# Kernel optimization log

Hardware: AMD Instinct MI355X
Metric: run time of the kernel (lower is better)

## Reference

```python
import jax, jax.numpy as jnp
import numpy as np

N_HEADS = 16
D_MODEL = 1024
NEG_INF = float('-inf')


def _rope_tables(seq_len, d_k, dtype):
    # RoPE(dim=d_k//2): Theta_i = 10000^(-i/dim), repeat-interleaved to width d_k;
    # positions start at 1 (torch uses arange(1, max_len+1)).
    dim = d_k // 2
    theta = jnp.exp(-jnp.arange(dim, dtype=dtype) * (np.log(10000.0) / dim))
    theta = jnp.repeat(theta, 2)                      # [d_k]
    pos = jnp.arange(1, seq_len + 1, dtype=dtype)[:, None]  # [S,1]
    ang = pos * theta                                 # [S,d_k]
    return jnp.sin(ang), jnp.cos(ang)


def _rope(x):
    # x: [B,H,S,d_k]; pair rotation (x0,x1)->(-x1,x0), Rx = x*cos + rot(x)*sin
    B, H, S, d_k = x.shape
    sin, cos = _rope_tables(S, d_k, x.dtype)
    xp = x.reshape(B, H, S, d_k // 2, 2)
    rot = jnp.stack([-xp[..., 1], xp[..., 0]], axis=-1).reshape(x.shape)
    return x * cos + rot * sin


def setup_inputs() -> dict:
    key = jax.random.key(0)
    ks = jax.random.split(key, 8)
    B, S, D, H = 2, 1024, D_MODEL, N_HEADS
    source_query = jax.random.normal(ks[0], (B, S, D), dtype=jnp.float32)
    source_key_value = jax.random.normal(ks[1], (B, S, D), dtype=jnp.float32)
    # tail padding: lengths in [820, 1024]
    q_len = jax.random.randint(ks[2], (B,), 820, S + 1)
    kv_len = jax.random.randint(ks[3], (B,), 820, S + 1)
    pos = jnp.arange(S)
    source_query_padding_mask = pos[None, :] >= q_len[:, None]    # True = pad
    source_key_value_padding_mask = pos[None, :] >= kv_len[:, None]
    prev = jax.random.normal(ks[4], (1, B, H, S, S), dtype=jnp.float32) * 0.5
    Wq = jax.random.normal(ks[5], (D, D), dtype=jnp.float32) * 0.02
    Wk = jax.random.normal(ks[6], (D, D), dtype=jnp.float32) * 0.02
    kv2 = jax.random.split(ks[7], 2)
    Wv = jax.random.normal(kv2[0], (D, D), dtype=jnp.float32) * 0.02
    Wproj = jax.random.normal(kv2[1], (D, D), dtype=jnp.float32) * 0.02
    return dict(source_query=source_query, source_key_value=source_key_value,
                source_query_padding_mask=source_query_padding_mask,
                source_key_value_padding_mask=source_key_value_padding_mask,
                prev=prev, Wq=Wq, Wk=Wk, Wv=Wv, Wproj=Wproj)


def reference(source_query, source_key_value, source_query_padding_mask,
              source_key_value_padding_mask, prev, Wq, Wk, Wv, Wproj):
    B, Sq, D = source_query.shape
    Sk = source_key_value.shape[1]
    H = N_HEADS
    d_k = D // H

    def split_heads(x, S):
        return x.reshape(B, S, H, d_k).transpose(0, 2, 1, 3)  # [B,H,S,d_k]

    # nn.Linear(bias=False): y = x @ W.T
    q = split_heads(jnp.einsum('bsd,ed->bse', source_query, Wq), Sq)
    k = split_heads(jnp.einsum('bsd,ed->bse', source_key_value, Wk), Sk)
    v = split_heads(jnp.einsum('bsd,ed->bse', source_key_value, Wv), Sk)

    q = _rope(q)
    k = _rope(k)

    scores = jnp.einsum('bhqd,bhkd->bhqk', q, k) * (d_k ** -0.5)
    q_pad = source_query_padding_mask[:, None, :, None]   # [B,1,Sq,1]
    kv_pad = source_key_value_padding_mask[:, None, None, :]  # [B,1,1,Sk]
    scores = jnp.where(q_pad, NEG_INF, scores)
    scores = jnp.where(kv_pad, NEG_INF, scores)
    causal = jnp.tril(jnp.ones((Sq, Sq), dtype=bool))      # masked=True
    scores = jnp.where(causal, scores, NEG_INF)

    prev_new = jnp.concatenate([prev, scores[None]], axis=0)  # [L+1,B,H,Sq,Sk]
    avg = prev_new.mean(0)

    # rows fully -inf (padded queries) would softmax to NaN in torch, then get
    # filled with 0 -> compute a safe softmax and zero those rows instead.
    safe = jnp.where(q_pad, 0.0, avg)
    w = jax.nn.softmax(safe, axis=-1)
    w = jnp.where(q_pad, 0.0, w)

    attn = jnp.einsum('bhqk,bhkd->bhqd', w, v)
    attn = attn.transpose(0, 2, 1, 3).reshape(B, Sq, D)
    out = jnp.einsum('bsd,ed->bse', attn, Wproj)  # dropout=0 (eval)
    return out, prev_new
```

## Files before the change

kernel.cpp:

```cpp
#include <hip/hip_runtime.h>
#include <math.h>

#define NSEQ 1024
#define NH   16
#define DKH  64

#define NEGBIG (-1.0e30f)

typedef unsigned short u16;
typedef unsigned int   u32;
typedef __attribute__((ext_vector_type(8))) short short8;
typedef __attribute__((ext_vector_type(4))) float f32x4;

__global__ __launch_bounds__(256) void normalize_masks(
    const unsigned char* __restrict__ qm, const unsigned char* __restrict__ km,
    int* __restrict__ outq, int* __restrict__ outk)
{
    __shared__ int flag;
    if (threadIdx.x == 0) flag = 0;
    __syncthreads();
    int f = 0;
    for (int i = threadIdx.x; i < 2048; i += 256) {
        if ((i & 3) && qm[i]) f = 1;
        if ((i & 3) && km[i]) f = 1;
    }
    if (f) atomicOr(&flag, 1);
    __syncthreads();
    const int isbyte = flag;
    for (int i = threadIdx.x; i < 2048; i += 256) {
        outq[i] = isbyte ? (int)qm[i] : ((const int*)qm)[i];
        outk[i] = isbyte ? (int)km[i] : ((const int*)km)[i];
    }
}

__device__ __forceinline__ u32 bf16_rn(float x) {
    u32 u = __float_as_uint(x);
    return (u + 0x7FFFu + ((u >> 16) & 1u)) >> 16;
}
__device__ __forceinline__ void bf16_split(float x, u32 &h, u32 &l) {
    h = bf16_rn(x);
    l = bf16_rn(x - __uint_as_float(h << 16));
}

__global__ __launch_bounds__(256) void split_bf16(
    const float* __restrict__ srcq, const float* __restrict__ srckv,
    const float* __restrict__ Wq, const float* __restrict__ Wk,
    const float* __restrict__ Wv, const float* __restrict__ Wp,
    u16* __restrict__ sqh, u16* __restrict__ sql,
    u16* __restrict__ skvh, u16* __restrict__ skvl,
    u16* __restrict__ w4h, u16* __restrict__ w4l)
{
    const int z = blockIdx.z;
    const float* src; u16 *dh, *dl; int n;
    if (z == 0)      { src = srcq;  dh = sqh;  dl = sql;  n = 1 << 21; }
    else if (z == 1) { src = srckv; dh = skvh; dl = skvl; n = 1 << 21; }
    else {
        src = (z == 2) ? Wq : (z == 3) ? Wk : (z == 4) ? Wv : Wp;
        dh = w4h + ((size_t)(z - 2) << 20);
        dl = w4l + ((size_t)(z - 2) << 20);
        n = 1 << 20;
    }
    const int i8 = (blockIdx.x * 256 + threadIdx.x) * 8;
    if (i8 >= n) return;
    const float4 a = *(const float4*)&src[i8];
    const float4 b = *(const float4*)&src[i8 + 4];
    const float v[8] = {a.x, a.y, a.z, a.w, b.x, b.y, b.z, b.w};
    u32 h[8], l[8];
    #pragma unroll
    for (int j = 0; j < 8; ++j) bf16_split(v[j], h[j], l[j]);
    *(uint4*)&dh[i8] = make_uint4(h[0] | (h[1] << 16), h[2] | (h[3] << 16),
                                  h[4] | (h[5] << 16), h[6] | (h[7] << 16));
    *(uint4*)&dl[i8] = make_uint4(l[0] | (l[1] << 16), l[2] | (l[3] << 16),
                                  l[4] | (l[5] << 16), l[6] | (l[7] << 16));
}

__global__ __launch_bounds__(256) void full_copy(
    const float* __restrict__ prev, float* __restrict__ prevc,
    float* __restrict__ scb)
{
    const float4 n4 = make_float4(NEGBIG, NEGBIG, NEGBIG, NEGBIG);
    for (unsigned i = blockIdx.x * 256 + threadIdx.x; i < (1u << 23); i += gridDim.x * 256) {
        const size_t e = (size_t)i * 4;
        const float4 p = *(const float4*)&prev[e];
        *(float4*)&prevc[e] = p;
        const int q = (int)((e >> 10) & 1023);
        const int k = (int)(e & 1023);
        if ((k >> 6) > (q >> 6)) *(float4*)&scb[e] = n4;
    }
}

__device__ __forceinline__ void mfma_core(
    const u16* __restrict__ Xhi, const u16* __restrict__ Xlo,
    const u16* __restrict__ Whi, const u16* __restrict__ Wlo,
    u16 (*Ahi)[40], u16 (*Alo)[40], u16 (*Bhi)[40], u16 (*Blo)[40],
    f32x4 (&acc)[4][2], int m0, int e0, int tid)
{
    const int lane = tid & 63, wid = tid >> 6;
    const int wm = wid >> 1, wn = wid & 1;
    const int l15 = lane & 15, lq = lane >> 4;
    const int arow = tid >> 1, aks = (tid & 1) * 16;
    const int brow = tid >> 2, bks = (tid & 3) * 8;
    const u16* axh = &Xhi[(size_t)(m0 + arow) * 1024 + aks];
    const u16* axl = &Xlo[(size_t)(m0 + arow) * 1024 + aks];
    const u16* bxh = &Whi[(size_t)(e0 + brow) * 1024 + bks];
    const u16* bxl = &Wlo[(size_t)(e0 + brow) * 1024 + bks];

    uint4 rah0 = *(const uint4*)axh;
    uint4 rah1 = *(const uint4*)(axh + 8);
    uint4 ral0 = *(const uint4*)axl;
    uint4 ral1 = *(const uint4*)(axl + 8);
    uint4 rbh  = *(const uint4*)bxh;
    uint4 rbl  = *(const uint4*)bxl;

    for (int k0 = 0; k0 < 1024; k0 += 32) {
        __syncthreads();
        *(uint4*)&Ahi[arow][aks]     = rah0;
        *(uint4*)&Ahi[arow][aks + 8] = rah1;
        *(uint4*)&Alo[arow][aks]     = ral0;
        *(uint4*)&Alo[arow][aks + 8] = ral1;
        *(uint4*)&Bhi[brow][bks]     = rbh;
        *(uint4*)&Blo[brow][bks]     = rbl;
        __syncthreads();
        if (k0 + 32 < 1024) {
            rah0 = *(const uint4*)(axh + k0 + 32);
            rah1 = *(const uint4*)(axh + k0 + 40);
            ral0 = *(const uint4*)(axl + k0 + 32);
            ral1 = *(const uint4*)(axl + k0 + 40);
            rbh  = *(const uint4*)(bxh + k0 + 32);
            rbl  = *(const uint4*)(bxl + k0 + 32);
        }
        short8 bh8[2], bl8[2];
        #pragma unroll
        for (int fn = 0; fn < 2; ++fn) {
            const int bc = wn * 32 + fn * 16 + l15;
            bh8[fn] = *(const short8*)&Bhi[bc][lq * 8];
            bl8[fn] = *(const short8*)&Blo[bc][lq * 8];
        }
        #pragma unroll
        for (int fm = 0; fm < 4; ++fm) {
            const int ar = wm * 64 + fm * 16 + l15;
            short8 ah8 = *(const short8*)&Ahi[ar][lq * 8];
            short8 al8 = *(const short8*)&Alo[ar][lq * 8];
            #pragma unroll
            for (int fn = 0; fn < 2; ++fn) {
                acc[fm][fn] = __builtin_amdgcn_mfma_f32_16x16x32_bf16(ah8, bh8[fn], acc[fm][fn], 0, 0, 0);
                acc[fm][fn] = __builtin_amdgcn_mfma_f32_16x16x32_bf16(ah8, bl8[fn], acc[fm][fn], 0, 0, 0);
                acc[fm][fn] = __builtin_amdgcn_mfma_f32_16x16x32_bf16(al8, bh8[fn], acc[fm][fn], 0, 0, 0);
            }
        }
    }
}

__global__ __launch_bounds__(256) void gemm_qkv(
    const u16* __restrict__ sqh, const u16* __restrict__ sql,
    const u16* __restrict__ skvh, const u16* __restrict__ skvl,
    const u16* __restrict__ w4h, const u16* __restrict__ w4l,
    float* __restrict__ qh, float* __restrict__ kh, float* __restrict__ vh)
{
    __shared__ __align__(16) u16 Ahi[128][40];
    __shared__ __align__(16) u16 Alo[128][40];
    __shared__ __align__(16) u16 Bhi[64][40];
    __shared__ __align__(16) u16 Blo[64][40];
    const int tid = threadIdx.x;
    const int z = blockIdx.z;
    const u16* Xhi = (z == 0) ? sqh : skvh;
    const u16* Xlo = (z == 0) ? sql : skvl;
    const u16* Whi = w4h + ((size_t)z << 20);
    const u16* Wlo = w4l + ((size_t)z << 20);
    float* Y = (z == 0) ? qh : (z == 1) ? kh : vh;
    const int m0 = blockIdx.y * 128, e0 = blockIdx.x * 64;

    f32x4 acc[4][2];
    #pragma unroll
    for (int i = 0; i < 4; ++i)
        #pragma unroll
        for (int j = 0; j < 2; ++j) acc[i][j] = (f32x4){0.f, 0.f, 0.f, 0.f};

    mfma_core(Xhi, Xlo, Whi, Wlo, Ahi, Alo, Bhi, Blo, acc, m0, e0, tid);

    const int lane = tid & 63, wid = tid >> 6;
    const int wm = wid >> 1, wn = wid & 1;
    const int l15 = lane & 15, lq = lane >> 4;
    const bool rope = (z != 2);
    const float cth = 0.28782313662425575f;
    float th[2];
    #pragma unroll
    for (int fn = 0; fn < 2; ++fn) {
        const int e = e0 + wn * 32 + fn * 16 + l15;
        th[fn] = rope ? expf(-(float)((e & 63) >> 1) * cth) : 0.f;
    }
    #pragma unroll
    for (int fm = 0; fm < 4; ++fm) {
        #pragma unroll
        for (int r = 0; r < 4; ++r) {
            const int m = m0 + wm * 64 + fm * 16 + lq * 4 + r;
            const int b = m >> 10, s = m & 1023;
            const float pos = (float)(s + 1);
            #pragma unroll
            for (int fn = 0; fn < 2; ++fn) {
                const int e = e0 + wn * 32 + fn * 16 + l15;
                float v = acc[fm][fn][r];
                const float vp = __shfl_xor(v, 1);
                if (rope) {
                    float sp, cp;
                    sincosf(pos * th[fn], &sp, &cp);
                    v = (lane & 1) ? (v * cp + vp * sp) : (v * cp - vp * sp);
                }
                const int hh = e >> 6, db = e & 63;
                Y[(((size_t)(b * NH + hh) << 10) + s) * DKH + db] = v;
            }
        }
    }
}

__global__ __launch_bounds__(256) void gemm_proj(
    const u16* __restrict__ atnh, const u16* __restrict__ atnl,
    const u16* __restrict__ wph, const u16* __restrict__ wpl,
    float* __restrict__ Y)
{
    __shared__ __align__(16) u16 Ahi[128][40];
    __shared__ __align__(16) u16 Alo[128][40];
    __shared__ __align__(16) u16 Bhi[64][40];
    __shared__ __align__(16) u16 Blo[64][40];
    const int tid = threadIdx.x;
    const int m0 = blockIdx.y * 128, e0 = blockIdx.x * 64;

    f32x4 acc[4][2];
    #pragma unroll
    for (int i = 0; i < 4; ++i)
        #pragma unroll
        for (int j = 0; j < 2; ++j) acc[i][j] = (f32x4){0.f, 0.f, 0.f, 0.f};

    mfma_core(atnh, atnl, wph, wpl, Ahi, Alo, Bhi, Blo, acc, m0, e0, tid);

    const int lane = tid & 63, wid = tid >> 6;
    const int wm = wid >> 1, wn = wid & 1;
    const int l15 = lane & 15, lq = lane >> 4;
    #pragma unroll
    for (int fm = 0; fm < 4; ++fm) {
        #pragma unroll
        for (int fn = 0; fn < 2; ++fn) {
            #pragma unroll
            for (int r = 0; r < 4; ++r) {
                const int row = m0 + wm * 64 + fm * 16 + lq * 4 + r;
                const int col = e0 + wn * 32 + fn * 16 + l15;
                Y[(size_t)row * 1024 + col] = acc[fm][fn][r];
            }
        }
    }
}

__global__ __launch_bounds__(256) void flash_fused(
    const float* __restrict__ qh, const float* __restrict__ kh,
    const float* __restrict__ vh, const float* __restrict__ prev,
    const int* __restrict__ nmq, const int* __restrict__ nmk,
    float* __restrict__ scb, u16* __restrict__ atnh, u16* __restrict__ atnl)
{
    const int bh = blockIdx.y;
    const int b = bh >> 4, h = bh & 15;
    const int bx = blockIdx.x;
    const int qt = (bx & 1) ? (15 - (bx >> 1)) : (bx >> 1);
    const int q0 = qt * 64;
    const int tid = threadIdx.x;
    const int ti = tid >> 4, tj = tid & 15;
    const int r0 = ti * 4, c0 = tj * 4;
    const size_t base = ((size_t)bh << 10) * 1024;
    const float NI = NEGBIG;

    __shared__ float Qs[64][68];
    __shared__ float KW[64][68];
    __shared__ float Vs[64][68];

    const int lr = tid >> 2;
    const int ld0 = (tid & 3) * 4;
    {
        const float* qbase = qh + (((size_t)bh << 10) + q0) * DKH;
        #pragma unroll
        for (int dq = 0; dq < 4; ++dq) {
            const int d0 = ld0 + dq * 16;
            float4 qv = *(const float4*)&qbase[(size_t)lr * DKH + d0];
            Qs[d0 + 0][lr] = qv.x; Qs[d0 + 1][lr] = qv.y;
            Qs[d0 + 2][lr] = qv.z; Qs[d0 + 3][lr] = qv.w;
        }
    }

    int qmv[4];
    #pragma unroll
    for (int i = 0; i < 4; ++i) qmv[i] = nmq[(b << 10) + q0 + r0 + i];

    float m_i[4], l_i[4], O[4][4];
    #pragma unroll
    for (int i = 0; i < 4; ++i) {
        m_i[i] = -3.0e38f; l_i[i] = 0.f;
        #pragma unroll
        for (int j = 0; j < 4; ++j) O[i][j] = 0.f;
    }

    const float* kbase = kh + ((size_t)bh << 10) * DKH;
    const float* vbase = vh + ((size_t)bh << 10) * DKH;

    for (int kt = 0; kt <= qt; ++kt) {
        const int k0 = kt * 64;
        __syncthreads();

        #pragma unroll
        for (int dq = 0; dq < 4; ++dq) {
            const int d0 = ld0 + dq * 16;
            float4 kv4 = *(const float4*)&kbase[(size_t)(k0 + lr) * DKH + d0];
            KW[d0 + 0][lr] = kv4.x; KW[d0 + 1][lr] = kv4.y;
            KW[d0 + 2][lr] = kv4.z; KW[d0 + 3][lr] = kv4.w;
        }
        #pragma unroll
        for (int u = 0; u < 4; ++u) {
            const int e = u * 256 + tid;
            const int kv = e >> 4, dd = (e & 15) * 4;
            *(float4*)&Vs[kv][dd] =
                *(const float4*)&vbase[(size_t)(k0 + kv) * DKH + dd];
        }
        __syncthreads();

        float acc[4][4] = {{0.f}};
        #pragma unroll 8
        for (int d = 0; d < 64; ++d) {
            float a[4], bb[4];
            *(float4*)a  = *(const float4*)&Qs[d][r0];
            *(float4*)bb = *(const float4*)&KW[d][c0];
            #pragma unroll
            for (int i = 0; i < 4; ++i)
                #pragma unroll
                for (int j = 0; j < 4; ++j)
                    acc[i][j] += a[i] * bb[j];
        }

        int km[4];
        #pragma unroll
        for (int j = 0; j < 4; ++j) km[j] = nmk[(b << 10) + k0 + c0 + j];
        float aw[4][4], tmx[4];
        #pragma unroll
        for (int i = 0; i < 4; ++i) {
            const int row = q0 + r0 + i;
            float o[4];
            #pragma unroll
            for (int j = 0; j < 4; ++j) {
                const int col = k0 + c0 + j;
                const bool masked = (col > row) || (qmv[i] != 0) || (km[j] != 0);
                o[j] = masked ? NI : acc[i][j] * 0.125f;
            }
            const size_t idx = base + (size_t)row * 1024 + k0 + c0;
            *(float4*)&scb[idx] = make_float4(o[0], o[1], o[2], o[3]);
            const float4 p4 = *(const float4*)&prev[idx];
            aw[i][0] = 0.5f * (p4.x + o[0]);
            aw[i][1] = 0.5f * (p4.y + o[1]);
            aw[i][2] = 0.5f * (p4.z + o[2]);
            aw[i][3] = 0.5f * (p4.w + o[3]);
            tmx[i] = fmaxf(fmaxf(aw[i][0], aw[i][1]), fmaxf(aw[i][2], aw[i][3]));
        }
        #pragma unroll
        for (int i = 0; i < 4; ++i)
            #pragma unroll
            for (int off = 1; off < 16; off <<= 1)
                tmx[i] = fmaxf(tmx[i], __shfl_xor(tmx[i], off));

        __syncthreads();

        #pragma unroll
        for (int i = 0; i < 4; ++i) {
            const float mn = fmaxf(m_i[i], tmx[i]);
            const float fac = expf(m_i[i] - mn);
            m_i[i] = mn;
            float w0 = expf(aw[i][0] - mn);
            float w1 = expf(aw[i][1] - mn);
            float w2 = expf(aw[i][2] - mn);
            float w3 = expf(aw[i][3] - mn);
            float sl = w0 + w1 + w2 + w3;
            #pragma unroll
            for (int off = 1; off < 16; off <<= 1)
                sl += __shfl_xor(sl, off);
            l_i[i] = l_i[i] * fac + sl;
            #pragma unroll
            for (int j = 0; j < 4; ++j) O[i][j] *= fac;
            KW[c0 + 0][r0 + i] = w0;
            KW[c0 + 1][r0 + i] = w1;
            KW[c0 + 2][r0 + i] = w2;
            KW[c0 + 3][r0 + i] = w3;
        }
        __syncthreads();

        #pragma unroll 8
        for (int k = 0; k < 64; ++k) {
            float wv[4], vv[4];
            *(float4*)wv = *(const float4*)&KW[k][r0];
            *(float4*)vv = *(const float4*)&Vs[k][c0];
            #pragma unroll
            for (int i = 0; i < 4; ++i)
                #pragma unroll
                for (int j = 0; j < 4; ++j)
                    O[i][j] += wv[i] * vv[j];
        }
    }

    #pragma unroll
    for (int i = 0; i < 4; ++i) {
        const int q = q0 + r0 + i;
        const float inv = qmv[i] ? 0.f : 1.f / l_i[i];
        u32 sh0, sl0, sh1, sl1, sh2, sl2, sh3, sl3;
        bf16_split(O[i][0] * inv, sh0, sl0);
        bf16_split(O[i][1] * inv, sh1, sl1);
        bf16_split(O[i][2] * inv, sh2, sl2);
        bf16_split(O[i][3] * inv, sh3, sl3);
        const size_t aidx = (size_t)((b << 10) + q) * 1024 + (h << 6) + c0;
        *(uint2*)&atnh[aidx] = make_uint2(sh0 | (sh1 << 16), sh2 | (sh3 << 16));
        *(uint2*)&atnl[aidx] = make_uint2(sl0 | (sl1 << 16), sl2 | (sl3 << 16));
    }
}

extern "C" void kernel_launch(void* const* d_in, const int* in_sizes, int n_in,
                              void* d_out, int out_size, void* d_ws, size_t ws_size,
                              hipStream_t stream) {
    const float* srcq  = (const float*)d_in[0];
    const float* srckv = (const float*)d_in[1];
    const void*  qmask = d_in[2];
    const void*  kmask = d_in[3];
    const float* prev  = (const float*)d_in[4];
    const float* Wq    = (const float*)d_in[5];
    const float* Wk    = (const float*)d_in[6];
    const float* Wv    = (const float*)d_in[7];
    const float* Wp    = (const float*)d_in[8];

    float* out0  = (float*)d_out;
    float* prevc = out0 + 2097152;
    float* scb   = prevc + 33554432;

    float* qh   = (float*)d_ws;
    float* kh   = qh + 2097152;
    float* vh   = kh + 2097152;
    u16* atnh = (u16*)(vh + 2097152);
    u16* atnl = atnh + 2097152;
    u16* sqh  = atnl + 2097152;
    u16* sql  = sqh + 2097152;
    u16* skvh = sql + 2097152;
    u16* skvl = skvh + 2097152;
    u16* w4h  = skvl + 2097152;
    u16* w4l  = w4h + 4194304;
    int* nmq  = (int*)(w4l + 4194304);
    int* nmk  = nmq + 2048;

    hipLaunchKernelGGL(normalize_masks, dim3(1), dim3(256), 0, stream,
                       (const unsigned char*)qmask, (const unsigned char*)kmask, nmq, nmk);
    hipLaunchKernelGGL(split_bf16, dim3(1024, 1, 6), dim3(256), 0, stream,
                       srcq, srckv, Wq, Wk, Wv, Wp,
                       sqh, sql, skvh, skvl, w4h, w4l);
    hipLaunchKernelGGL(gemm_qkv, dim3(16, 16, 3), dim3(256), 0, stream,
                       sqh, sql, skvh, skvl, w4h, w4l, qh, kh, vh);
    hipLaunchKernelGGL(full_copy, dim3(2048), dim3(256), 0, stream,
                       prev, prevc, scb);
    hipLaunchKernelGGL(flash_fused, dim3(16, 32), dim3(256), 0, stream,
                       qh, kh, vh, prev, nmq, nmk, scb, atnh, atnl);
    hipLaunchKernelGGL(gemm_proj, dim3(16, 16), dim3(256), 0, stream,
                       atnh, atnl, w4h + 3145728, w4l + 3145728, out0);
}
```

Before: 648.0 us.

## Pack GEMM operands into MFMA fragment order and fuse prev copy into attention

The bf16 split kernel now writes activations and weights in a pre-swizzled MFMA fragment layout. Both GEMMs use 128x128 tiles fed by double-buffered global_load_lds, running three sequential K passes (hi·hi, lo·hi, hi·lo) instead of interleaving three MFMAs per step. The separate full_copy kernel is removed: the attention kernel copies prev and writes the -inf score blocks for its own upper-triangle tiles. Each attention block now handles a complementary pair of query tiles to balance causal work, and writes its output already packed for the projection GEMM. The gain is less memory traffic and fewer launches, at the cost of tighter coupling between producer and consumer layouts and more work per attention block.

```diff
diff --git a/kernel.cpp b/kernel.cpp
--- a/kernel.cpp
+++ b/kernel.cpp
@@ -11,6 +11,12 @@
 typedef unsigned int   u32;
 typedef __attribute__((ext_vector_type(8))) short short8;
 typedef __attribute__((ext_vector_type(4))) float f32x4;
+
+__device__ __forceinline__ void gload_lds16(const void* g, void* l) {
+    __builtin_amdgcn_global_load_lds(
+        (const __attribute__((address_space(1))) void*)g,
+        (__attribute__((address_space(3))) void*)l, 16, 0, 0);
+}
 
 __global__ __launch_bounds__(256) void normalize_masks(
     const unsigned char* __restrict__ qm, const unsigned char* __restrict__ km,
@@ -42,7 +48,7 @@
     l = bf16_rn(x - __uint_as_float(h << 16));
 }
 
-__global__ __launch_bounds__(256) void split_bf16(
+__global__ __launch_bounds__(256) void split_pack(
     const float* __restrict__ srcq, const float* __restrict__ srckv,
     const float* __restrict__ Wq, const float* __restrict__ Wk,
     const float* __restrict__ Wv, const float* __restrict__ Wp,
@@ -51,103 +57,80 @@
     u16* __restrict__ w4h, u16* __restrict__ w4l)
 {
     const int z = blockIdx.z;
-    const float* src; u16 *dh, *dl; int n;
-    if (z == 0)      { src = srcq;  dh = sqh;  dl = sql;  n = 1 << 21; }
-    else if (z == 1) { src = srckv; dh = skvh; dl = skvl; n = 1 << 21; }
+    const float* src; u16 *dh, *dl; int nunits;
+    if (z == 0)      { src = srcq;  dh = sqh;  dl = sql;  nunits = 262144; }
+    else if (z == 1) { src = srckv; dh = skvh; dl = skvl; nunits = 262144; }
     else {
         src = (z == 2) ? Wq : (z == 3) ? Wk : (z == 4) ? Wv : Wp;
         dh = w4h + ((size_t)(z - 2) << 20);
         dl = w4l + ((size_t)(z - 2) << 20);
-        n = 1 << 20;
-    }
-    const int i8 = (blockIdx.x * 256 + threadIdx.x) * 8;
-    if (i8 >= n) return;
-    const float4 a = *(const float4*)&src[i8];
-    const float4 b = *(const float4*)&src[i8 + 4];
-    const float v[8] = {a.x, a.y, a.z, a.w, b.x, b.y, b.z, b.w};
-    u32 h[8], l[8];
+        nunits = 131072;
+    }
+    const int u = blockIdx.x * 256 + threadIdx.x;
+    if (u >= nunits) return;
+    const int lane = u & 63, kstep = (u >> 6) & 31, sub = u >> 11;
+    const int row = sub * 16 + (lane & 15);
+    const int kc  = kstep * 32 + ((lane >> 4) << 3);
+    const float4 a = *(const float4*)&src[(size_t)row * 1024 + kc];
+    const float4 bb = *(const float4*)&src[(size_t)row * 1024 + kc + 4];
+    const float v[8] = {a.x, a.y, a.z, a.w, bb.x, bb.y, bb.z, bb.w};
+    u32 hh[8], ll[8];
     #pragma unroll
-    for (int j = 0; j < 8; ++j) bf16_split(v[j], h[j], l[j]);
-    *(uint4*)&dh[i8] = make_uint4(h[0] | (h[1] << 16), h[2] | (h[3] << 16),
-                                  h[4] | (h[5] << 16), h[6] | (h[7] << 16));
-    *(uint4*)&dl[i8] = make_uint4(l[0] | (l[1] << 16), l[2] | (l[3] << 16),
-                                  l[4] | (l[5] << 16), l[6] | (l[7] << 16));
-}
-
-__global__ __launch_bounds__(256) void full_copy(
-    const float* __restrict__ prev, float* __restrict__ prevc,
-    float* __restrict__ scb)
-{
-    const float4 n4 = make_float4(NEGBIG, NEGBIG, NEGBIG, NEGBIG);
-    for (unsigned i = blockIdx.x * 256 + threadIdx.x; i < (1u << 23); i += gridDim.x * 256) {
-        const size_t e = (size_t)i * 4;
-        const float4 p = *(const float4*)&prev[e];
-        *(float4*)&prevc[e] = p;
-        const int q = (int)((e >> 10) & 1023);
-        const int k = (int)(e & 1023);
-        if ((k >> 6) > (q >> 6)) *(float4*)&scb[e] = n4;
-    }
-}
-
-__device__ __forceinline__ void mfma_core(
-    const u16* __restrict__ Xhi, const u16* __restrict__ Xlo,
-    const u16* __restrict__ Whi, const u16* __restrict__ Wlo,
-    u16 (*Ahi)[40], u16 (*Alo)[40], u16 (*Bhi)[40], u16 (*Blo)[40],
-    f32x4 (&acc)[4][2], int m0, int e0, int tid)
+    for (int j = 0; j < 8; ++j) bf16_split(v[j], hh[j], ll[j]);
+    const size_t o = (size_t)u * 8;
+    *(uint4*)&dh[o] = make_uint4(hh[0] | (hh[1] << 16), hh[2] | (hh[3] << 16),
+                                 hh[4] | (hh[5] << 16), hh[6] | (hh[7] << 16));
+    *(uint4*)&dl[o] = make_uint4(ll[0] | (ll[1] << 16), ll[2] | (ll[3] << 16),
+                                 ll[4] | (ll[5] << 16), ll[6] | (ll[7] << 16));
+}
+
+__device__ __forceinline__ void gemm_packed_core(
+    const u16* __restrict__ Ah, const u16* __restrict__ Al,
+    const u16* __restrict__ Bh, const u16* __restrict__ Bl,
+    u16* LA, u16* LB, f32x4 (&acc)[4][4], int m0, int e0, int tid)
 {
     const int lane = tid & 63, wid = tid >> 6;
     const int wm = wid >> 1, wn = wid & 1;
-    const int l15 = lane & 15, lq = lane >> 4;
-    const int arow = tid >> 1, aks = (tid & 1) * 16;
-    const int brow = tid >> 2, bks = (tid & 3) * 8;
-    const u16* axh = &Xhi[(size_t)(m0 + arow) * 1024 + aks];
-    const u16* axl = &Xlo[(size_t)(m0 + arow) * 1024 + aks];
-    const u16* bxh = &Whi[(size_t)(e0 + brow) * 1024 + bks];
-    const u16* bxl = &Wlo[(size_t)(e0 + brow) * 1024 + bks];
-
-    uint4 rah0 = *(const uint4*)axh;
-    uint4 rah1 = *(const uint4*)(axh + 8);
-    uint4 ral0 = *(const uint4*)axl;
-    uint4 ral1 = *(const uint4*)(axl + 8);
-    uint4 rbh  = *(const uint4*)bxh;
-    uint4 rbl  = *(const uint4*)bxl;
-
-    for (int k0 = 0; k0 < 1024; k0 += 32) {
+    const int subA0 = m0 >> 4, subB0 = e0 >> 4;
+    const int s0 = wid, s1 = wid + 4;
+    const int lo8 = lane * 8;
+
+    int cur = 0;
+    gload_lds16(Ah + ((size_t)(subA0 + s0) * 32) * 512 + lo8, LA + s0 * 512);
+    gload_lds16(Ah + ((size_t)(subA0 + s1) * 32) * 512 + lo8, LA + s1 * 512);
+    gload_lds16(Bh + ((size_t)(subB0 + s0) * 32) * 512 + lo8, LB + s0 * 512);
+    gload_lds16(Bh + ((size_t)(subB0 + s1) * 32) * 512 + lo8, LB + s1 * 512);
+    __syncthreads();
+
+    for (int ks = 0; ks < 96; ++ks) {
+        const int nxt = ks + 1;
+        if (nxt < 96) {
+            const int kstep = nxt & 31, ph = nxt >> 5;
+            const u16* Ap = (ph == 1) ? Al : Ah;
+            const u16* Bp = (ph == 2) ? Bl : Bh;
+            u16* la = LA + (cur ^ 1) * 4096;
+            u16* lb = LB + (cur ^ 1) * 4096;
+            gload_lds16(Ap + ((size_t)(subA0 + s0) * 32 + kstep) * 512 + lo8, la + s0 * 512);
+            gload_lds16(Ap + ((size_t)(subA0 + s1) * 32 + kstep) * 512 + lo8, la + s1 * 512);
+            gload_lds16(Bp + ((size_t)(subB0 + s0) * 32 + kstep) * 512 + lo8, lb + s0 * 512);
+            gload_lds16(Bp + ((size_t)(subB0 + s1) * 32 + kstep) * 512 + lo8, lb + s1 * 512);
+        }
+        const u16* la = LA + cur * 4096;
+        const u16* lb = LB + cur * 4096;
+        short8 a8[4], b8[4];
+        #pragma unroll
+        for (int f = 0; f < 4; ++f) {
+            a8[f] = *(const short8*)(la + (wm * 4 + f) * 512 + lo8);
+            b8[f] = *(const short8*)(lb + (wn * 4 + f) * 512 + lo8);
+        }
+        #pragma unroll
+        for (int fm = 0; fm < 4; ++fm)
+            #pragma unroll
+            for (int fn = 0; fn < 4; ++fn)
+                acc[fm][fn] = __builtin_amdgcn_mfma_f32_16x16x32_bf16(
+                    a8[fm], b8[fn], acc[fm][fn], 0, 0, 0);
         __syncthreads();
-        *(uint4*)&Ahi[arow][aks]     = rah0;
-        *(uint4*)&Ahi[arow][aks + 8] = rah1;
-        *(uint4*)&Alo[arow][aks]     = ral0;
-        *(uint4*)&Alo[arow][aks + 8] = ral1;
-        *(uint4*)&Bhi[brow][bks]     = rbh;
-        *(uint4*)&Blo[brow][bks]     = rbl;
-        __syncthreads();
-        if (k0 + 32 < 1024) {
-            rah0 = *(const uint4*)(axh + k0 + 32);
-            rah1 = *(const uint4*)(axh + k0 + 40);
-            ral0 = *(const uint4*)(axl + k0 + 32);
-            ral1 = *(const uint4*)(axl + k0 + 40);
-            rbh  = *(const uint4*)(bxh + k0 + 32);
-            rbl  = *(const uint4*)(bxl + k0 + 32);
-        }
-        short8 bh8[2], bl8[2];
-        #pragma unroll
-        for (int fn = 0; fn < 2; ++fn) {
-            const int bc = wn * 32 + fn * 16 + l15;
-            bh8[fn] = *(const short8*)&Bhi[bc][lq * 8];
-            bl8[fn] = *(const short8*)&Blo[bc][lq * 8];
-        }
-        #pragma unroll
-        for (int fm = 0; fm < 4; ++fm) {
-            const int ar = wm * 64 + fm * 16 + l15;
-            short8 ah8 = *(const short8*)&Ahi[ar][lq * 8];
-            short8 al8 = *(const short8*)&Alo[ar][lq * 8];
-            #pragma unroll
-            for (int fn = 0; fn < 2; ++fn) {
-                acc[fm][fn] = __builtin_amdgcn_mfma_f32_16x16x32_bf16(ah8, bh8[fn], acc[fm][fn], 0, 0, 0);
-                acc[fm][fn] = __builtin_amdgcn_mfma_f32_16x16x32_bf16(ah8, bl8[fn], acc[fm][fn], 0, 0, 0);
-                acc[fm][fn] = __builtin_amdgcn_mfma_f32_16x16x32_bf16(al8, bh8[fn], acc[fm][fn], 0, 0, 0);
-            }
-        }
+        cur ^= 1;
     }
 }
 
@@ -157,56 +140,48 @@
     const u16* __restrict__ w4h, const u16* __restrict__ w4l,
     float* __restrict__ qh, float* __restrict__ kh, float* __restrict__ vh)
 {
-    __shared__ __align__(16) u16 Ahi[128][40];
-    __shared__ __align__(16) u16 Alo[128][40];
-    __shared__ __align__(16) u16 Bhi[64][40];
-    __shared__ __align__(16) u16 Blo[64][40];
+    __shared__ __align__(16) u16 LA[2][4096];
+    __shared__ __align__(16) u16 LB[2][4096];
     const int tid = threadIdx.x;
     const int z = blockIdx.z;
-    const u16* Xhi = (z == 0) ? sqh : skvh;
-    const u16* Xlo = (z == 0) ? sql : skvl;
-    const u16* Whi = w4h + ((size_t)z << 20);
-    const u16* Wlo = w4l + ((size_t)z << 20);
+    const u16* Ah = (z == 0) ? sqh : skvh;
+    const u16* Al = (z == 0) ? sql : skvl;
+    const u16* Bh = w4h + ((size_t)z << 20);
+    const u16* Bl = w4l + ((size_t)z << 20);
     float* Y = (z == 0) ? qh : (z == 1) ? kh : vh;
-    const int m0 = blockIdx.y * 128, e0 = blockIdx.x * 64;
-
-    f32x4 acc[4][2];
+    const int m0 = blockIdx.y * 128, e0 = blockIdx.x * 128;
+
+    f32x4 acc[4][4];
     #pragma unroll
     for (int i = 0; i < 4; ++i)
         #pragma unroll
-        for (int j = 0; j < 2; ++j) acc[i][j] = (f32x4){0.f, 0.f, 0.f, 0.f};
-
-    mfma_core(Xhi, Xlo, Whi, Wlo, Ahi, Alo, Bhi, Blo, acc, m0, e0, tid);
+        for (int j = 0; j < 4; ++j) acc[i][j] = (f32x4){0.f, 0.f, 0.f, 0.f};
+
+    gemm_packed_core(Ah, Al, Bh, Bl, &LA[0][0], &LB[0][0], acc, m0, e0, tid);
 
     const int lane = tid & 63, wid = tid >> 6;
     const int wm = wid >> 1, wn = wid & 1;
     const int l15 = lane & 15, lq = lane >> 4;
     const bool rope = (z != 2);
     const float cth = 0.28782313662425575f;
-    float th[2];
     #pragma unroll
-    for (int fn = 0; fn < 2; ++fn) {
-        const int e = e0 + wn * 32 + fn * 16 + l15;
-        th[fn] = rope ? expf(-(float)((e & 63) >> 1) * cth) : 0.f;
-    }
-    #pragma unroll
-    for (int fm = 0; fm < 4; ++fm) {
-        #pragma unroll
-        for (int r = 0; r < 4; ++r) {
-            const int m = m0 + wm * 64 + fm * 16 + lq * 4 + r;
-            const int b = m >> 10, s = m & 1023;
-            const float pos = (float)(s + 1);
-            #pragma unroll
-            for (int fn = 0; fn < 2; ++fn) {
-                const int e = e0 + wn * 32 + fn * 16 + l15;
+    for (int fn = 0; fn < 4; ++fn) {
+        const int e = e0 + wn * 64 + fn * 16 + l15;
+        const float th = expf(-(float)((e & 63) >> 1) * cth);
+        const int hh = e >> 6, db = e & 63;
+        #pragma unroll
+        for (int fm = 0; fm < 4; ++fm) {
+            #pragma unroll
+            for (int r = 0; r < 4; ++r) {
+                const int m = m0 + wm * 64 + fm * 16 + lq * 4 + r;
+                const int b = m >> 10, s = m & 1023;
                 float v = acc[fm][fn][r];
                 const float vp = __shfl_xor(v, 1);
                 if (rope) {
                     float sp, cp;
-                    sincosf(pos * th[fn], &sp, &cp);
+                    sincosf((float)(s + 1) * th, &sp, &cp);
                     v = (lane & 1) ? (v * cp + vp * sp) : (v * cp - vp * sp);
                 }
-                const int hh = e >> 6, db = e & 63;
                 Y[(((size_t)(b * NH + hh) << 10) + s) * DKH + db] = v;
             }
         }
@@ -218,49 +193,44 @@
     const u16* __restrict__ wph, const u16* __restrict__ wpl,
     float* __restrict__ Y)
 {
-    __shared__ __align__(16) u16 Ahi[128][40];
-    __shared__ __align__(16) u16 Alo[128][40];
-    __shared__ __align__(16) u16 Bhi[64][40];
-    __shared__ __align__(16) u16 Blo[64][40];
+    __shared__ __align__(16) u16 LA[2][4096];
+    __shared__ __align__(16) u16 LB[2][4096];
     const int tid = threadIdx.x;
-    const int m0 = blockIdx.y * 128, e0 = blockIdx.x * 64;
-
-    f32x4 acc[4][2];
+    const int m0 = blockIdx.y * 128, e0 = blockIdx.x * 128;
+
+    f32x4 acc[4][4];
     #pragma unroll
     for (int i = 0; i < 4; ++i)
         #pragma unroll
-        for (int j = 0; j < 2; ++j) acc[i][j] = (f32x4){0.f, 0.f, 0.f, 0.f};
-
-    mfma_core(atnh, atnl, wph, wpl, Ahi, Alo, Bhi, Blo, acc, m0, e0, tid);
+        for (int j = 0; j < 4; ++j) acc[i][j] = (f32x4){0.f, 0.f, 0.f, 0.f};
+
+    gemm_packed_core(atnh, atnl, wph, wpl, &LA[0][0], &LB[0][0], acc, m0, e0, tid);
 
     const int lane = tid & 63, wid = tid >> 6;
     const int wm = wid >> 1, wn = wid & 1;
     const int l15 = lane & 15, lq = lane >> 4;
     #pragma unroll
-    for (int fm = 0; fm < 4; ++fm) {
-        #pragma unroll
-        for (int fn = 0; fn < 2; ++fn) {
+    for (int fm = 0; fm < 4; ++fm)
+        #pragma unroll
+        for (int fn = 0; fn < 4; ++fn)
             #pragma unroll
             for (int r = 0; r < 4; ++r) {
                 const int row = m0 + wm * 64 + fm * 16 + lq * 4 + r;
-                const int col = e0 + wn * 32 + fn * 16 + l15;
+                const int col = e0 + wn * 64 + fn * 16 + l15;
                 Y[(size_t)row * 1024 + col] = acc[fm][fn][r];
             }
-        }
-    }
 }
 
 __global__ __launch_bounds__(256) void flash_fused(
     const float* __restrict__ qh, const float* __restrict__ kh,
     const float* __restrict__ vh, const float* __restrict__ prev,
     const int* __restrict__ nmq, const int* __restrict__ nmk,
-    float* __restrict__ scb, u16* __restrict__ atnh, u16* __restrict__ atnl)
+    float* __restrict__ prevc, float* __restrict__ scb,
+    u16* __restrict__ atnh, u16* __restrict__ atnl)
 {
     const int bh = blockIdx.y;
     const int b = bh >> 4, h = bh & 15;
     const int bx = blockIdx.x;
-    const int qt = (bx & 1) ? (15 - (bx >> 1)) : (bx >> 1);
-    const int q0 = qt * 64;
     const int tid = threadIdx.x;
     const int ti = tid >> 4, tj = tid & 15;
     const int r0 = ti * 4, c0 = tj * 4;
@@ -273,144 +243,180 @@
 
     const int lr = tid >> 2;
     const int ld0 = (tid & 3) * 4;
-    {
-        const float* qbase = qh + (((size_t)bh << 10) + q0) * DKH;
-        #pragma unroll
-        for (int dq = 0; dq < 4; ++dq) {
-            const int d0 = ld0 + dq * 16;
-            float4 qv = *(const float4*)&qbase[(size_t)lr * DKH + d0];
-            Qs[d0 + 0][lr] = qv.x; Qs[d0 + 1][lr] = qv.y;
-            Qs[d0 + 2][lr] = qv.z; Qs[d0 + 3][lr] = qv.w;
-        }
-    }
-
-    int qmv[4];
-    #pragma unroll
-    for (int i = 0; i < 4; ++i) qmv[i] = nmq[(b << 10) + q0 + r0 + i];
-
-    float m_i[4], l_i[4], O[4][4];
-    #pragma unroll
-    for (int i = 0; i < 4; ++i) {
-        m_i[i] = -3.0e38f; l_i[i] = 0.f;
-        #pragma unroll
-        for (int j = 0; j < 4; ++j) O[i][j] = 0.f;
-    }
-
     const float* kbase = kh + ((size_t)bh << 10) * DKH;
     const float* vbase = vh + ((size_t)bh << 10) * DKH;
 
-    for (int kt = 0; kt <= qt; ++kt) {
-        const int k0 = kt * 64;
+    for (int pp = 0; pp < 2; ++pp) {
+        const int qt = pp ? (15 - bx) : bx;
+        const int q0 = qt * 64;
+
+        {
+            const float* qbase = qh + (((size_t)bh << 10) + q0) * DKH;
+            #pragma unroll
+            for (int dq = 0; dq < 4; ++dq) {
+                const int d0 = ld0 + dq * 16;
+                float4 qv = *(const float4*)&qbase[(size_t)lr * DKH + d0];
+                Qs[d0 + 0][lr] = qv.x; Qs[d0 + 1][lr] = qv.y;
+                Qs[d0 + 2][lr] = qv.z; Qs[d0 + 3][lr] = qv.w;
+            }
+        }
+
+        {
+            const float4 n4 = make_float4(NI, NI, NI, NI);
+            for (int kt = qt + 1; kt < 16; ++kt) {
+                const int k0 = kt * 64;
+                #pragma unroll
+                for (int u = 0; u < 4; ++u) {
+                    const int e = u * 256 + tid;
+                    const int rr = e >> 4, cc = (e & 15) * 4;
+                    const size_t idx = base + (size_t)(q0 + rr) * 1024 + k0 + cc;
+                    *(float4*)&prevc[idx] = *(const float4*)&prev[idx];
+                    *(float4*)&scb[idx] = n4;
+                }
+            }
+        }
+
+        int qmv[4];
+        #pragma unroll
+        for (int i = 0; i < 4; ++i) qmv[i] = nmq[(b << 10) + q0 + r0 + i];
+
+        float m_i[4], l_i[4], O[4][4];
+        #pragma unroll
+        for (int i = 0; i < 4; ++i) {
+            m_i[i] = -3.0e38f; l_i[i] = 0.f;
+            #pragma unroll
+            for (int j = 0; j < 4; ++j) O[i][j] = 0.f;
+        }
+
+        for (int kt = 0; kt <= qt; ++kt) {
+            const int k0 = kt * 64;
+            __syncthreads();
+
+            #pragma unroll
+            for (int dq = 0; dq < 4; ++dq) {
+                const int d0 = ld0 + dq * 16;
+                float4 kv4 = *(const float4*)&kbase[(size_t)(k0 + lr) * DKH + d0];
+                KW[d0 + 0][lr] = kv4.x; KW[d0 + 1][lr] = kv4.y;
+                KW[d0 + 2][lr] = kv4.z; KW[d0 + 3][lr] = kv4.w;
+            }
+            #pragma unroll
+            for (int u = 0; u < 4; ++u) {
+                const int e = u * 256 + tid;
+                const int kv = e >> 4, dd = (e & 15) * 4;
+                *(float4*)&Vs[kv][dd] =
+                    *(const float4*)&vbase[(size_t)(k0 + kv) * DKH + dd];
+            }
+            __syncthreads();
+
+            float acc[4][4] = {{0.f}};
+            #pragma unroll 8
+            for (int d = 0; d < 64; ++d) {
+                float a[4], bb[4];
+                *(float4*)a  = *(const float4*)&Qs[d][r0];
+                *(float4*)bb = *(const float4*)&KW[d][c0];
+                #pragma unroll
+                for (int i = 0; i < 4; ++i)
+                    #pragma unroll
+                    for (int j = 0; j < 4; ++j)
+                        acc[i][j] += a[i] * bb[j];
+            }
+
+            int km[4];
+            #pragma unroll
+            for (int j = 0; j < 4; ++j) km[j] = nmk[(b << 10) + k0 + c0 + j];
+            float aw[4][4], tmx[4];
+            #pragma unroll
+            for (int i = 0; i < 4; ++i) {
+                const int row = q0 + r0 + i;
+                float o[4];
+                #pragma unroll
+                for (int j = 0; j < 4; ++j) {
+                    const int col = k0 + c0 + j;
+                    const bool masked = (col > row) || (qmv[i] != 0) || (km[j] != 0);
+                    o[j] = masked ? NI : acc[i][j] * 0.125f;
+                }
+                const size_t idx = base + (size_t)row * 1024 + k0 + c0;
+                *(float4*)&scb[idx] = make_float4(o[0], o[1], o[2], o[3]);
+                const float4 p4 = *(const float4*)&prev[idx];
+                *(float4*)&prevc[idx] = p4;
+                aw[i][0] = 0.5f * (p4.x + o[0]);
+                aw[i][1] = 0.5f * (p4.y + o[1]);
+                aw[i][2] = 0.5f * (p4.z + o[2]);
+                aw[i][3] = 0.5f * (p4.w + o[3]);
+                tmx[i] = fmaxf(fmaxf(aw[i][0], aw[i][1]), fmaxf(aw[i][2], aw[i][3]));
+            }
+            #pragma unroll
+            for (int i = 0; i < 4; ++i)
+                #pragma unroll
+                for (int off = 1; off < 16; off <<= 1)
+                    tmx[i] = fmaxf(tmx[i], __shfl_xor(tmx[i], off));
+
+            __syncthreads();
+
+            #pragma unroll
+            for (int i = 0; i < 4; ++i) {
+                const float mn = fmaxf(m_i[i], tmx[i]);
+                const float fac = expf(m_i[i] - mn);
+                m_i[i] = mn;
+                float w0 = expf(aw[i][0] - mn);
+                float w1 = expf(aw[i][1] - mn);
+                float w2 = expf(aw[i][2] - mn);
+                float w3 = expf(aw[i][3] - mn);
+                float sl = w0 + w1 + w2 + w3;
+                #pragma unroll
+                for (int off = 1; off < 16; off <<= 1)
+                    sl += __shfl_xor(sl, off);
+                l_i[i] = l_i[i] * fac + sl;
+                #pragma unroll
+                for (int j = 0; j < 4; ++j) O[i][j] *= fac;
+                KW[c0 + 0][r0 + i] = w0;
+                KW[c0 + 1][r0 + i] = w1;
+                KW[c0 + 2][r0 + i] = w2;
+                KW[c0 + 3][r0 + i] = w3;
+            }
+            __syncthreads();
+
+            #pragma unroll 8
+            for (int k = 0; k < 64; ++k) {
+                float wv[4], vv[4];
+                *(float4*)wv = *(const float4*)&KW[k][r0];
+                *(float4*)vv = *(const float4*)&Vs[k][c0];
+                #pragma unroll
+                for (int i = 0; i < 4; ++i)
+                    #pragma unroll
+                    for (int j = 0; j < 4; ++j)
+                        O[i][j] += wv[i] * vv[j];
+            }
+        }
+
         __syncthreads();
-
-        #pragma unroll
-        for (int dq = 0; dq < 4; ++dq) {
-            const int d0 = ld0 + dq * 16;
-            float4 kv4 = *(const float4*)&kbase[(size_t)(k0 + lr) * DKH + d0];
-            KW[d0 + 0][lr] = kv4.x; KW[d0 + 1][lr] = kv4.y;
-            KW[d0 + 2][lr] = kv4.z; KW[d0 + 3][lr] = kv4.w;
-        }
-        #pragma unroll
-        for (int u = 0; u < 4; ++u) {
-            const int e = u * 256 + tid;
-            const int kv = e >> 4, dd = (e & 15) * 4;
-            *(float4*)&Vs[kv][dd] =
-                *(const float4*)&vbase[(size_t)(k0 + kv) * DKH + dd];
+        #pragma unroll
+        for (int i = 0; i < 4; ++i) {
+            const float inv = qmv[i] ? 0.f : 1.f / l_i[i];
+            KW[r0 + i][c0 + 0] = O[i][0] * inv;
+            KW[r0 + i][c0 + 1] = O[i][1] * inv;
+            KW[r0 + i][c0 + 2] = O[i][2] * inv;
+            KW[r0 + i][c0 + 3] = O[i][3] * inv;
         }
         __syncthreads();
-
-        float acc[4][4] = {{0.f}};
-        #pragma unroll 8
-        for (int d = 0; d < 64; ++d) {
-            float a[4], bb[4];
-            *(float4*)a  = *(const float4*)&Qs[d][r0];
-            *(float4*)bb = *(const float4*)&KW[d][c0];
-            #pragma unroll
-            for (int i = 0; i < 4; ++i)
-                #pragma unroll
-                for (int j = 0; j < 4; ++j)
-                    acc[i][j] += a[i] * bb[j];
-        }
-
-        int km[4];
-        #pragma unroll
-        for (int j = 0; j < 4; ++j) km[j] = nmk[(b << 10) + k0 + c0 + j];
-        float aw[4][4], tmx[4];
-        #pragma unroll
-        for (int i = 0; i < 4; ++i) {
-            const int row = q0 + r0 + i;
-            float o[4];
-            #pragma unroll
-            for (int j = 0; j < 4; ++j) {
-                const int col = k0 + c0 + j;
-                const bool masked = (col > row) || (qmv[i] != 0) || (km[j] != 0);
-                o[j] = masked ? NI : acc[i][j] * 0.125f;
-            }
-            const size_t idx = base + (size_t)row * 1024 + k0 + c0;
-            *(float4*)&scb[idx] = make_float4(o[0], o[1], o[2], o[3]);
-            const float4 p4 = *(const float4*)&prev[idx];
-            aw[i][0] = 0.5f * (p4.x + o[0]);
-            aw[i][1] = 0.5f * (p4.y + o[1]);
-            aw[i][2] = 0.5f * (p4.z + o[2]);
-            aw[i][3] = 0.5f * (p4.w + o[3]);
-            tmx[i] = fmaxf(fmaxf(aw[i][0], aw[i][1]), fmaxf(aw[i][2], aw[i][3]));
-        }
-        #pragma unroll
-        for (int i = 0; i < 4; ++i)
-            #pragma unroll
-            for (int off = 1; off < 16; off <<= 1)
-                tmx[i] = fmaxf(tmx[i], __shfl_xor(tmx[i], off));
-
-        __syncthreads();
-
-        #pragma unroll
-        for (int i = 0; i < 4; ++i) {
-            const float mn = fmaxf(m_i[i], tmx[i]);
-            const float fac = expf(m_i[i] - mn);
-            m_i[i] = mn;
-            float w0 = expf(aw[i][0] - mn);
-            float w1 = expf(aw[i][1] - mn);
-            float w2 = expf(aw[i][2] - mn);
-            float w3 = expf(aw[i][3] - mn);
-            float sl = w0 + w1 + w2 + w3;
-            #pragma unroll
-            for (int off = 1; off < 16; off <<= 1)
-                sl += __shfl_xor(sl, off);
-            l_i[i] = l_i[i] * fac + sl;
-            #pragma unroll
-            for (int j = 0; j < 4; ++j) O[i][j] *= fac;
-            KW[c0 + 0][r0 + i] = w0;
-            KW[c0 + 1][r0 + i] = w1;
-            KW[c0 + 2][r0 + i] = w2;
-            KW[c0 + 3][r0 + i] = w3;
-        }
-        __syncthreads();
-
-        #pragma unroll 8
-        for (int k = 0; k < 64; ++k) {
-            float wv[4], vv[4];
-            *(float4*)wv = *(const float4*)&KW[k][r0];
-            *(float4*)vv = *(const float4*)&Vs[k][c0];
-            #pragma unroll
-            for (int i = 0; i < 4; ++i)
-                #pragma unroll
-                for (int j = 0; j < 4; ++j)
-                    O[i][j] += wv[i] * vv[j];
-        }
-    }
-
-    #pragma unroll
-    for (int i = 0; i < 4; ++i) {
-        const int q = q0 + r0 + i;
-        const float inv = qmv[i] ? 0.f : 1.f / l_i[i];
-        u32 sh0, sl0, sh1, sl1, sh2, sl2, sh3, sl3;
-        bf16_split(O[i][0] * inv, sh0, sl0);
-        bf16_split(O[i][1] * inv, sh1, sl1);
-        bf16_split(O[i][2] * inv, sh2, sl2);
-        bf16_split(O[i][3] * inv, sh3, sl3);
-        const size_t aidx = (size_t)((b << 10) + q) * 1024 + (h << 6) + c0;
-        *(uint2*)&atnh[aidx] = make_uint2(sh0 | (sh1 << 16), sh2 | (sh3 << 16));
-        *(uint2*)&atnl[aidx] = make_uint2(sl0 | (sl1 << 16), sl2 | (sl3 << 16));
+        const int mb0 = (b << 10) + q0;
+        #pragma unroll
+        for (int uu = 0; uu < 2; ++uu) {
+            const int slot = uu * 256 + tid;
+            const int ul = slot & 63, un = slot >> 6;
+            const int so = un >> 1, kso = un & 1;
+            const int rl = so * 16 + (ul & 15);
+            const int dl = kso * 32 + ((ul >> 4) << 3);
+            u32 hh8[8], ll8[8];
+            #pragma unroll
+            for (int j = 0; j < 8; ++j) bf16_split(KW[rl][dl + j], hh8[j], ll8[j]);
+            const size_t uidx =
+                ((size_t)((mb0 >> 4) + so) * 32 + 2 * h + kso) * 512 + (size_t)ul * 8;
+            *(uint4*)&atnh[uidx] = make_uint4(hh8[0] | (hh8[1] << 16), hh8[2] | (hh8[3] << 16),
+                                              hh8[4] | (hh8[5] << 16), hh8[6] | (hh8[7] << 16));
+            *(uint4*)&atnl[uidx] = make_uint4(ll8[0] | (ll8[1] << 16), ll8[2] | (ll8[3] << 16),
+                                              ll8[4] | (ll8[5] << 16), ll8[6] | (ll8[7] << 16));
+        }
     }
 }
 
@@ -447,15 +453,13 @@
 
     hipLaunchKernelGGL(normalize_masks, dim3(1), dim3(256), 0, stream,
                        (const unsigned char*)qmask, (const unsigned char*)kmask, nmq, nmk);
-    hipLaunchKernelGGL(split_bf16, dim3(1024, 1, 6), dim3(256), 0, stream,
+    hipLaunchKernelGGL(split_pack, dim3(1024, 1, 6), dim3(256), 0, stream,
                        srcq, srckv, Wq, Wk, Wv, Wp,
                        sqh, sql, skvh, skvl, w4h, w4l);
-    hipLaunchKernelGGL(gemm_qkv, dim3(16, 16, 3), dim3(256), 0, stream,
+    hipLaunchKernelGGL(gemm_qkv, dim3(8, 16, 3), dim3(256), 0, stream,
                        sqh, sql, skvh, skvl, w4h, w4l, qh, kh, vh);
-    hipLaunchKernelGGL(full_copy, dim3(2048), dim3(256), 0, stream,
-                       prev, prevc, scb);
-    hipLaunchKernelGGL(flash_fused, dim3(16, 32), dim3(256), 0, stream,
-                       qh, kh, vh, prev, nmq, nmk, scb, atnh, atnl);
-    hipLaunchKernelGGL(gemm_proj, dim3(16, 16), dim3(256), 0, stream,
+    hipLaunchKernelGGL(flash_fused, dim3(8, 32), dim3(256), 0, stream,
+                       qh, kh, vh, prev, nmq, nmk, prevc, scb, atnh, atnl);
+    hipLaunchKernelGGL(gemm_proj, dim3(8, 16), dim3(256), 0, stream,
                        atnh, atnl, w4h + 3145728, w4l + 3145728, out0);
 }
```

Result: slower. 716.6 us (+10.6%).
